# Optimization experiments

Measured on AMD Instinct MI355X. Metric: run time of the kernel, lower is better.

Reference implementation:

```python
import jax, jax.numpy as jnp
import numpy as np
from jax import lax

S = 1024  # input_size
G = 10    # grid_size
F = 5     # fiter_size -> 11x11 gaussian kernel
B = 8
C = 3


def _gauss(size, fwhm):
    x = np.arange(size, dtype=np.float64)
    y = x[:, None]
    c = size // 2
    g = np.exp(-4 * np.log(2) * ((x - c) ** 2 + (y - c) ** 2) / fwhm ** 2)
    return (g / g.sum()).astype(np.float32)


def setup_inputs() -> dict:
    key = jax.random.key(0)
    k1, k2, k3 = jax.random.split(key, 3)
    x = jax.random.normal(k1, (B, C, S, S), dtype=jnp.float32)
    offset_x = jax.random.normal(k2, (B, 1, G, G), dtype=jnp.float32)
    offset_y = jax.random.normal(k3, (B, 1, G, G), dtype=jnp.float32)
    weight = jnp.asarray(_gauss(2 * F + 1, F))[None, None]  # [1,1,11,11]
    return {"x": x, "offset_x": offset_x, "offset_y": offset_y,
            "weight": weight, "max_move": 50}


def reference(x, offset_x, offset_y, weight, max_move):
    max_offset = 2.0 * max_move / S

    def smooth(o):  # replication pad + 11x11 gaussian conv + scale + clamp
        p = jnp.pad(o, ((0, 0), (0, 0), (F, F), (F, F)), mode="edge")
        c = lax.conv_general_dilated(p, weight, (1, 1), "VALID",
                                     dimension_numbers=("NCHW", "OIHW", "NCHW"))
        return jnp.clip(c * max_offset, -max_offset, max_offset)

    g = jnp.concatenate([smooth(offset_x), smooth(offset_y)], axis=1)  # [B,2,G,G]

    # bilinear upsample G -> S (align_corners=False, like F.interpolate)
    src = jnp.maximum((jnp.arange(S, dtype=jnp.float32) + 0.5) * (G / S) - 0.5, 0.0)
    i0 = jnp.minimum(jnp.floor(src).astype(jnp.int32), G - 1)
    i1 = jnp.minimum(i0 + 1, G - 1)
    w = src - i0.astype(jnp.float32)
    g = g[:, :, i0, :] * (1 - w)[None, None, :, None] + g[:, :, i1, :] * w[None, None, :, None]
    g = g[:, :, :, i0] * (1 - w) + g[:, :, :, i1] * w  # [B,2,S,S]

    # P basis: channel 0 = x coord, channel 1 = y coord, scaled to [-1,1]
    lin = jnp.arange(S, dtype=jnp.float32) / (S - 1.0)
    P = jnp.stack([jnp.broadcast_to(lin[None, :], (S, S)),
                   jnp.broadcast_to(lin[:, None], (S, S))]) * 2.0 - 1.0
    grid = jnp.clip(g + P, -1.0, 1.0).transpose(0, 2, 3, 1)  # [B,S,S,2] (x,y)

    def gs(img, gr):  # grid_sample bilinear, zeros padding, align_corners=False
        ix = ((gr[..., 0] + 1.0) * S - 1.0) / 2.0
        iy = ((gr[..., 1] + 1.0) * S - 1.0) / 2.0
        x0 = jnp.floor(ix).astype(jnp.int32); x1 = x0 + 1
        y0 = jnp.floor(iy).astype(jnp.int32); y1 = y0 + 1
        wx = ix - x0.astype(ix.dtype)
        wy = iy - y0.astype(iy.dtype)

        def corner(yy, xx, wt):
            v = img[:, jnp.clip(yy, 0, S - 1), jnp.clip(xx, 0, S - 1)]  # [C,S,S]
            m = ((yy >= 0) & (yy < S) & (xx >= 0) & (xx < S)).astype(img.dtype)
            return v * (m * wt)

        return (corner(y0, x0, (1 - wy) * (1 - wx)) + corner(y0, x1, (1 - wy) * wx)
                + corner(y1, x0, wy * (1 - wx)) + corner(y1, x1, wy * wx))

    return jax.vmap(gs)(x, grid)
```

## Files before the change

kernel.cpp:

```cpp
#include <hip/hip_runtime.h>

#define SS 1024
#define GG 10
#define FF 5
#define BB 8
#define CC 3
#define KK (2 * FF + 1)

typedef float f32x2 __attribute__((ext_vector_type(2)));

__global__ __launch_bounds__(256) void rds_smooth_kernel(
    const float* __restrict__ ox, const float* __restrict__ oy,
    const float* __restrict__ w, const void* __restrict__ max_move_p,
    float* __restrict__ gs)
{
    int idx = blockIdx.x * 256 + threadIdx.x;
    if (idx >= BB * 2 * GG * GG) return;
    int j  = idx % GG;
    int i  = (idx / GG) % GG;
    int ch = (idx / (GG * GG)) % 2;
    int b  = idx / (2 * GG * GG);

    const float* o = (ch == 0 ? ox : oy) + b * GG * GG;

    int mi = *(const int*)max_move_p;
    float mv = (mi >= -100000 && mi <= 100000) ? (float)mi : __int_as_float(mi);
    float max_offset = 2.0f * mv / (float)SS;

    float acc = 0.0f;
    for (int u = 0; u < KK; ++u) {
        int yy = min(max(i + u - FF, 0), GG - 1);
        for (int v = 0; v < KK; ++v) {
            int xx = min(max(j + v - FF, 0), GG - 1);
            acc += o[yy * GG + xx] * w[u * KK + v];
        }
    }
    acc *= max_offset;
    acc = fminf(fmaxf(acc, -max_offset), max_offset);
    gs[idx] = acc;
}

__global__ __launch_bounds__(256, 2) void rds_deform_kernel(
    const float* __restrict__ x, const float* __restrict__ gs,
    float* __restrict__ out)
{
    int wg    = blockIdx.x;
    int xseg  = wg & 3;
    int ytile = (wg >> 2) & 255;
    int b     = wg >> 10;
    int tid   = threadIdx.x;
    int ybase = ytile << 2;
    int xc    = (xseg << 8) + tid;

    __shared__ float rowf[4][2][GG];

    const float GdS = (float)GG / (float)SS;

    if (tid < 80) {
        int p  = tid / 20;
        int r  = tid - p * 20;
        int ch = r / GG;
        int j  = r - ch * GG;
        int y  = ybase + p;
        float sy  = fmaxf(((float)y + 0.5f) * GdS - 0.5f, 0.0f);
        int   i0y = min((int)sy, GG - 1);
        int   i1y = min(i0y + 1, GG - 1);
        float wyu = sy - (float)i0y;
        const float* gb = gs + (b * 2 + ch) * GG * GG;
        rowf[p][ch][j] = gb[i0y * GG + j] + wyu * (gb[i1y * GG + j] - gb[i0y * GG + j]);
    }
    __syncthreads();

    float sx  = fmaxf(((float)xc + 0.5f) * GdS - 0.5f, 0.0f);
    int   i0x = min((int)sx, GG - 1);
    int   i1x = min(i0x + 1, GG - 1);
    float wxu = sx - (float)i0x;
    float pxc = (float)xc * (2.0f / (float)(SS - 1)) - 1.0f;

    int   oa[4], ob[4];
    float wxa[4], wxb[4];
    float wya[4], wyb[4];

    #pragma unroll
    for (int p = 0; p < 4; ++p) {
        float r0a = rowf[p][0][i0x], r0b = rowf[p][0][i1x];
        float r1a = rowf[p][1][i0x], r1b = rowf[p][1][i1x];
        float gxv = r0a + wxu * (r0b - r0a);
        float gyv = r1a + wxu * (r1b - r1a);

        float py  = (float)(ybase + p) * (2.0f / (float)(SS - 1)) - 1.0f;
        float gr0 = fminf(fmaxf(gxv + pxc, -1.0f), 1.0f);
        float gr1 = fminf(fmaxf(gyv + py,  -1.0f), 1.0f);

        float ix = gr0 * 512.0f + 511.5f;
        float iy = gr1 * 512.0f + 511.5f;

        int   x0 = (int)floorf(ix);
        int   y0 = (int)floorf(iy);
        int   y1 = y0 + 1;
        float wx = ix - (float)x0;
        float wy = iy - (float)y0;

        int bclamp = min(max(x0, 0), SS - 2);
        int d      = x0 - bclamp;
        wxa[p] = (d == 0) ? (1.0f - wx) : ((d < 0) ? wx : 0.0f);
        wxb[p] = (d == 0) ? wx          : ((d < 0) ? 0.0f : (1.0f - wx));

        float my0 = ((unsigned)y0 < (unsigned)SS) ? 1.0f : 0.0f;
        float my1 = ((unsigned)y1 < (unsigned)SS) ? 1.0f : 0.0f;
        wya[p] = (1.0f - wy) * my0;
        wyb[p] = wy * my1;

        int cy0 = min(max(y0, 0), SS - 1);
        int cy1 = min(max(y1, 0), SS - 1);
        oa[p] = cy0 * SS + bclamp;
        ob[p] = cy1 * SS + bclamp;
    }

    const float* xb = x + (size_t)b * CC * SS * SS;
    size_t obase = (((size_t)b * CC) * SS + ybase) * SS + xc;

    #pragma unroll
    for (int c = 0; c < CC; ++c) {
        const float* img = xb + (size_t)c * SS * SS;

        f32x2 A0, A1, A2, A3, B0, B1, B2, B3;
        asm volatile("global_load_dwordx2 %0, %1, off" : "=v"(A0) : "v"(img + oa[0]));
        asm volatile("global_load_dwordx2 %0, %1, off" : "=v"(A1) : "v"(img + oa[1]));
        asm volatile("global_load_dwordx2 %0, %1, off" : "=v"(A2) : "v"(img + oa[2]));
        asm volatile("global_load_dwordx2 %0, %1, off" : "=v"(A3) : "v"(img + oa[3]));
        asm volatile("global_load_dwordx2 %0, %1, off" : "=v"(B0) : "v"(img + ob[0]));
        asm volatile("global_load_dwordx2 %0, %1, off" : "=v"(B1) : "v"(img + ob[1]));
        asm volatile("global_load_dwordx2 %0, %1, off" : "=v"(B2) : "v"(img + ob[2]));
        asm volatile("global_load_dwordx2 %0, %1, off" : "=v"(B3) : "v"(img + ob[3]));
        asm volatile("s_waitcnt vmcnt(0)" ::: "memory");
        __builtin_amdgcn_sched_barrier(0);

        f32x2 A[4] = { A0, A1, A2, A3 };
        f32x2 B[4] = { B0, B1, B2, B3 };
        #pragma unroll
        for (int p = 0; p < 4; ++p) {
            float v = wya[p] * (A[p].x * wxa[p] + A[p].y * wxb[p])
                    + wyb[p] * (B[p].x * wxa[p] + B[p].y * wxb[p]);
            __builtin_nontemporal_store(
                v, out + obase + (size_t)c * SS * SS + (size_t)(p * SS));
        }
    }
}

extern "C" void kernel_launch(void* const* d_in, const int* in_sizes, int n_in,
                              void* d_out, int out_size, void* d_ws, size_t ws_size,
                              hipStream_t stream) {
    const float* x        = (const float*)d_in[0];
    const float* offset_x = (const float*)d_in[1];
    const float* offset_y = (const float*)d_in[2];
    const float* weight   = (const float*)d_in[3];
    const void*  max_move = d_in[4];
    float* out = (float*)d_out;
    float* gs  = (float*)d_ws;

    int n1 = BB * 2 * GG * GG;
    rds_smooth_kernel<<<(n1 + 255) / 256, 256, 0, stream>>>(
        offset_x, offset_y, weight, max_move, gs);

    int nblocks = BB * (SS / 4) * 4;
    rds_deform_kernel<<<nblocks, 256, 0, stream>>>(x, gs, out);
}
```

Measured before the change: 196.2 us.

## Process 32 rows per block and drop inline-asm gathers for compiler loads

Each workgroup now covers 32 output rows instead of 4, so there are 8x fewer blocks and the shared row-interpolation setup is amortized over more rows. The hand-written global_load_dwordx2 asm with explicit waitcnt is replaced by plain vector loads with 4-byte alignment, letting the compiler schedule them inside a partially unrolled row loop. Grid coordinates are recomputed per channel instead of being kept in registers. This trades extra ALU work and fewer blocks in flight for lower per-block overhead, and the memory-level parallelism now depends on the compiler's scheduling.

```diff
diff --git a/kernel.cpp b/kernel.cpp
--- a/kernel.cpp
+++ b/kernel.cpp
@@ -7,7 +7,7 @@
 #define CC 3
 #define KK (2 * FF + 1)
 
-typedef float f32x2 __attribute__((ext_vector_type(2)));
+typedef float f32x2 __attribute__((ext_vector_type(2), aligned(4)));
 
 __global__ __launch_bounds__(256) void rds_smooth_kernel(
     const float* __restrict__ ox, const float* __restrict__ oy,
@@ -46,19 +46,19 @@
 {
     int wg    = blockIdx.x;
     int xseg  = wg & 3;
-    int ytile = (wg >> 2) & 255;
-    int b     = wg >> 10;
+    int yt    = (wg >> 2) & 31;
+    int b     = wg >> 7;
     int tid   = threadIdx.x;
-    int ybase = ytile << 2;
+    int ybase = yt << 5;
     int xc    = (xseg << 8) + tid;
 
-    __shared__ float rowf[4][2][GG];
+    __shared__ float rowf[32][2][GG];
 
     const float GdS = (float)GG / (float)SS;
 
-    if (tid < 80) {
-        int p  = tid / 20;
-        int r  = tid - p * 20;
+    for (int k = tid; k < 32 * 2 * GG; k += 256) {
+        int p  = k / (2 * GG);
+        int r  = k - p * 2 * GG;
         int ch = r / GG;
         int j  = r - ch * GG;
         int y  = ybase + p;
@@ -77,73 +77,50 @@
     float wxu = sx - (float)i0x;
     float pxc = (float)xc * (2.0f / (float)(SS - 1)) - 1.0f;
 
-    int   oa[4], ob[4];
-    float wxa[4], wxb[4];
-    float wya[4], wyb[4];
+    const float* xb = x + (size_t)b * CC * SS * SS;
 
-    #pragma unroll
-    for (int p = 0; p < 4; ++p) {
-        float r0a = rowf[p][0][i0x], r0b = rowf[p][0][i1x];
-        float r1a = rowf[p][1][i0x], r1b = rowf[p][1][i1x];
-        float gxv = r0a + wxu * (r0b - r0a);
-        float gyv = r1a + wxu * (r1b - r1a);
-
-        float py  = (float)(ybase + p) * (2.0f / (float)(SS - 1)) - 1.0f;
-        float gr0 = fminf(fmaxf(gxv + pxc, -1.0f), 1.0f);
-        float gr1 = fminf(fmaxf(gyv + py,  -1.0f), 1.0f);
-
-        float ix = gr0 * 512.0f + 511.5f;
-        float iy = gr1 * 512.0f + 511.5f;
-
-        int   x0 = (int)floorf(ix);
-        int   y0 = (int)floorf(iy);
-        int   y1 = y0 + 1;
-        float wx = ix - (float)x0;
-        float wy = iy - (float)y0;
-
-        int bclamp = min(max(x0, 0), SS - 2);
-        int d      = x0 - bclamp;
-        wxa[p] = (d == 0) ? (1.0f - wx) : ((d < 0) ? wx : 0.0f);
-        wxb[p] = (d == 0) ? wx          : ((d < 0) ? 0.0f : (1.0f - wx));
-
-        float my0 = ((unsigned)y0 < (unsigned)SS) ? 1.0f : 0.0f;
-        float my1 = ((unsigned)y1 < (unsigned)SS) ? 1.0f : 0.0f;
-        wya[p] = (1.0f - wy) * my0;
-        wyb[p] = wy * my1;
-
-        int cy0 = min(max(y0, 0), SS - 1);
-        int cy1 = min(max(y1, 0), SS - 1);
-        oa[p] = cy0 * SS + bclamp;
-        ob[p] = cy1 * SS + bclamp;
-    }
-
-    const float* xb = x + (size_t)b * CC * SS * SS;
-    size_t obase = (((size_t)b * CC) * SS + ybase) * SS + xc;
-
-    #pragma unroll
     for (int c = 0; c < CC; ++c) {
         const float* img = xb + (size_t)c * SS * SS;
+        float* op = out + ((size_t)(b * CC + c) * SS + ybase) * SS + xc;
 
-        f32x2 A0, A1, A2, A3, B0, B1, B2, B3;
-        asm volatile("global_load_dwordx2 %0, %1, off" : "=v"(A0) : "v"(img + oa[0]));
-        asm volatile("global_load_dwordx2 %0, %1, off" : "=v"(A1) : "v"(img + oa[1]));
-        asm volatile("global_load_dwordx2 %0, %1, off" : "=v"(A2) : "v"(img + oa[2]));
-        asm volatile("global_load_dwordx2 %0, %1, off" : "=v"(A3) : "v"(img + oa[3]));
-        asm volatile("global_load_dwordx2 %0, %1, off" : "=v"(B0) : "v"(img + ob[0]));
-        asm volatile("global_load_dwordx2 %0, %1, off" : "=v"(B1) : "v"(img + ob[1]));
-        asm volatile("global_load_dwordx2 %0, %1, off" : "=v"(B2) : "v"(img + ob[2]));
-        asm volatile("global_load_dwordx2 %0, %1, off" : "=v"(B3) : "v"(img + ob[3]));
-        asm volatile("s_waitcnt vmcnt(0)" ::: "memory");
-        __builtin_amdgcn_sched_barrier(0);
+        #pragma unroll 4
+        for (int p = 0; p < 32; ++p) {
+            float r0a = rowf[p][0][i0x], r0b = rowf[p][0][i1x];
+            float r1a = rowf[p][1][i0x], r1b = rowf[p][1][i1x];
+            float gxv = r0a + wxu * (r0b - r0a);
+            float gyv = r1a + wxu * (r1b - r1a);
 
-        f32x2 A[4] = { A0, A1, A2, A3 };
-        f32x2 B[4] = { B0, B1, B2, B3 };
-        #pragma unroll
-        for (int p = 0; p < 4; ++p) {
-            float v = wya[p] * (A[p].x * wxa[p] + A[p].y * wxb[p])
-                    + wyb[p] * (B[p].x * wxa[p] + B[p].y * wxb[p]);
-            __builtin_nontemporal_store(
-                v, out + obase + (size_t)c * SS * SS + (size_t)(p * SS));
+            float py  = (float)(ybase + p) * (2.0f / (float)(SS - 1)) - 1.0f;
+            float gr0 = fminf(fmaxf(gxv + pxc, -1.0f), 1.0f);
+            float gr1 = fminf(fmaxf(gyv + py,  -1.0f), 1.0f);
+
+            float ix = gr0 * 512.0f + 511.5f;
+            float iy = gr1 * 512.0f + 511.5f;
+
+            int   x0 = (int)floorf(ix);
+            int   y0 = (int)floorf(iy);
+            int   y1 = y0 + 1;
+            float wx = ix - (float)x0;
+            float wy = iy - (float)y0;
+
+            int bclamp = min(max(x0, 0), SS - 2);
+            int d      = x0 - bclamp;
+            float wxa = (d == 0) ? (1.0f - wx) : ((d < 0) ? wx : 0.0f);
+            float wxb = (d == 0) ? wx          : ((d < 0) ? 0.0f : (1.0f - wx));
+
+            float my0 = ((unsigned)y0 < (unsigned)SS) ? 1.0f : 0.0f;
+            float my1 = ((unsigned)y1 < (unsigned)SS) ? 1.0f : 0.0f;
+            float wya = (1.0f - wy) * my0;
+            float wyb = wy * my1;
+
+            int cy0 = min(max(y0, 0), SS - 1);
+            int cy1 = min(max(y1, 0), SS - 1);
+
+            f32x2 A = *(const f32x2*)(img + cy0 * SS + bclamp);
+            f32x2 B = *(const f32x2*)(img + cy1 * SS + bclamp);
+            float v = wya * (A.x * wxa + A.y * wxb)
+                    + wyb * (B.x * wxa + B.y * wxb);
+            __builtin_nontemporal_store(v, op + (size_t)p * SS);
         }
     }
 }
@@ -163,6 +140,6 @@
     rds_smooth_kernel<<<(n1 + 255) / 256, 256, 0, stream>>>(
         offset_x, offset_y, weight, max_move, gs);
 
-    int nblocks = BB * (SS / 4) * 4;
+    int nblocks = BB * (SS / 32) * 4;
     rds_deform_kernel<<<nblocks, 256, 0, stream>>>(x, gs, out);
 }
```

Result: slower. 203.7 us (+3.9%).
